# Performance work log

Hardware: AMD Instinct MI355X
Metric: run time of the kernel (lower is better)

## Reference

```python
import jax, jax.numpy as jnp
import numpy as np

B, IN, OUT = 8192, 4096, 2048  # OUT must equal 32*64 per betta/gamma sizes


def setup_inputs() -> dict:
    key = jax.random.key(0)
    kx, kw = jax.random.split(key, 2)
    X = jax.random.normal(kx, (B, IN), dtype=jnp.float32)
    # xavier-uniform-like init for W
    limit = float(np.sqrt(6.0 / (IN + OUT)))
    W = jax.random.uniform(kw, (IN, OUT), minval=-limit, maxval=limit, dtype=jnp.float32)
    absmean = jnp.abs(W).mean(axis=0)
    alpha = jnp.abs(W).mean()          # scalar, >= 0
    betta = absmean[:32]               # (32,), >= 0
    gamma = absmean[32:96]             # (64,), >= 0
    return {"X": X, "W": W, "alpha": alpha, "betta": betta, "gamma": gamma}


def reference(X, W, alpha, betta, gamma):
    # module applies relu_ to alpha/betta/gamma data before the functional call
    alpha = jax.nn.relu(alpha)
    betta = jax.nn.relu(betta)
    gamma = jax.nn.relu(gamma)
    X_bin = jnp.sign(X)                # (B, IN)
    W_bin = jnp.sign(W)                # (IN, OUT)
    # scale[i*64+j] = alpha * betta[i] * gamma[j] -> (OUT,)
    scale = (alpha * jnp.outer(betta, gamma)).reshape(-1)
    return (X_bin @ W_bin) * scale     # (B, OUT)
```

## Files before the change

kernel.cpp:

```cpp
#include <hip/hip_runtime.h>


#define M_DIM 8192
#define K_DIM 4096
#define N_DIM 2048
#define NT    (K_DIM / 256)
#define TILE_BYTES 32768
#define PANEL_BYTES (NT * TILE_BYTES)

typedef int i32x4 __attribute__((ext_vector_type(4)));
typedef int i32x8 __attribute__((ext_vector_type(8)));
typedef float f32x16 __attribute__((ext_vector_type(16)));

__device__ __forceinline__ unsigned int nib4(float x) {
  unsigned int s = (__float_as_uint(x) >> 28) & 0x8u;
  return x == 0.0f ? 0u : (0x2u | s);
}

__device__ __forceinline__ unsigned int pack8(const float* f) {
  unsigned int p = 0;
#pragma unroll
  for (int j = 0; j < 8; ++j) p |= nib4(f[j]) << (4 * j);
  return p;
}

__device__ __forceinline__ void gload_lds16(const void* g, void* lds) {
  __builtin_amdgcn_global_load_lds(
      (const __attribute__((address_space(1))) unsigned int*)g,
      (__attribute__((address_space(3))) unsigned int*)lds, 16, 0, 0);
}

__device__ __forceinline__ i32x8 pad8(i32x4 v) {
  i32x8 r;
  r[0] = v[0]; r[1] = v[1]; r[2] = v[2]; r[3] = v[3];
  r[4] = 0; r[5] = 0; r[6] = 0; r[7] = 0;
  return r;
}

__global__ __launch_bounds__(256) void binX_kernel(
    const float* __restrict__ X, unsigned char* __restrict__ Xq) {
  __shared__ float tile[32][260];
  const int t = threadIdx.x;
  const int rg = blockIdx.x >> 4;
  const int kt = blockIdx.x & 15;
  const int lrow = t >> 6;
  const int col4 = (t & 63) * 4;
#pragma unroll
  for (int i = 0; i < 8; ++i)
    *(float4*)&tile[i * 4 + lrow][col4] =
        *(const float4*)&X[(size_t)(rg * 32 + i * 4 + lrow) * K_DIM + kt * 256 + col4];
  __syncthreads();
  const int s = t >> 5;
  const int r = t & 31;
  float f[32];
#pragma unroll
  for (int j = 0; j < 32; ++j) f[j] = tile[r][s * 32 + j];
  uint4 gq;
  gq.x = pack8(f + 0);  gq.y = pack8(f + 8);
  gq.z = pack8(f + 16); gq.w = pack8(f + 24);
  const int row = rg * 32 + r;
  unsigned char* dst = Xq + (size_t)(row >> 8) * PANEL_BYTES + kt * TILE_BYTES +
                       ((size_t)s * 256 + (row & 255)) * 16;
  *(uint4*)dst = gq;
}

__global__ __launch_bounds__(256) void binW_kernel(
    const float* __restrict__ W, unsigned char* __restrict__ Wq) {
  __shared__ float tile[32][260];
  const int t = threadIdx.x;
  const int q = blockIdx.x >> 7;
  const int kt = (blockIdx.x >> 3) & 15;
  const int s = blockIdx.x & 7;
#pragma unroll
  for (int i = 0; i < 8; ++i) {
    int row = i * 4 + (t >> 6);
    int col4 = (t & 63) * 4;
    *(float4*)&tile[row][col4] =
        *(const float4*)&W[(size_t)(kt * 256 + s * 32 + row) * N_DIM + q * 256 + col4];
  }
  __syncthreads();
  float f[32];
#pragma unroll
  for (int k = 0; k < 32; ++k) f[k] = tile[k][t];
  uint4 gq;
  gq.x = pack8(f + 0);  gq.y = pack8(f + 8);
  gq.z = pack8(f + 16); gq.w = pack8(f + 24);
  unsigned char* dst = Wq + (size_t)q * PANEL_BYTES + kt * TILE_BYTES +
                       ((size_t)s * 256 + t) * 16;
  *(uint4*)dst = gq;
}

__device__ __forceinline__ void stage_tile(const unsigned char* __restrict__ src,
                                           unsigned char* lds, int t) {
#pragma unroll
  for (int p = 0; p < 4; ++p) {
    int c = p * 512 + t;
    gload_lds16(src + c * 16, lds + c * 16);
  }
}

__device__ __forceinline__ void load_frags(i32x4* a4, i32x4* b4,
                                           const unsigned char* pA,
                                           const unsigned char* pB,
                                           int g, int wr, int wc, int l31) {
#pragma unroll
  for (int fm = 0; fm < 4; ++fm)
    a4[fm] = *(const i32x4*)&pA[(g * 256 + wr * 128 + fm * 32 + l31) * 16];
#pragma unroll
  for (int fn = 0; fn < 2; ++fn)
    b4[fn] = *(const i32x4*)&pB[(g * 256 + wc * 64 + fn * 32 + l31) * 16];
}

__global__ __launch_bounds__(512, 2) void gemm_fp4_kernel(
    const unsigned char* __restrict__ Aq,
    const unsigned char* __restrict__ Bq,
    const float* __restrict__ alpha,
    const float* __restrict__ betta,
    const float* __restrict__ gamma,
    float* __restrict__ C) {
  __shared__ __align__(16) unsigned char smem[131072];

  const int t = threadIdx.x;
  const int lane = t & 63;
  const int l31 = lane & 31;
  const int lhi = lane >> 5;
  const int w = t >> 6;
  const int wr = w >> 2;
  const int wc = w & 3;

  const int bid = blockIdx.x;
  const int bm = (bid & 7) * 4 + (bid >> 6);
  const int bn = (bid >> 3) & 7;
  const int row0 = bm * 256;
  const int col0 = bn * 256;

  const unsigned char* Abase = Aq + (size_t)bm * PANEL_BYTES;
  const unsigned char* Bbase = Bq + (size_t)bn * PANEL_BYTES;

  f32x16 acc[4][2];
#pragma unroll
  for (int fm = 0; fm < 4; ++fm)
#pragma unroll
    for (int fn = 0; fn < 2; ++fn)
#pragma unroll
      for (int r = 0; r < 16; ++r) acc[fm][fn][r] = 0.f;

  stage_tile(Abase, &smem[0], t);
  stage_tile(Bbase, &smem[32768], t);
  asm volatile("s_waitcnt vmcnt(0)" ::: "memory");
  __builtin_amdgcn_s_barrier();

  i32x4 a4[2][4], b4[2][2];
  load_frags(a4[0], b4[0], &smem[0], &smem[32768], lhi, wr, wc, l31);

  for (int kt = 0; kt < NT; ++kt) {
    const int cur = kt & 1;
    const unsigned char* pA = &smem[cur * 65536];
    const unsigned char* pB = pA + 32768;

#pragma unroll
    for (int kk = 0; kk < 4; ++kk) {
      const int pb = kk & 1, pn = pb ^ 1;
      asm volatile("s_waitcnt lgkmcnt(0)" ::: "memory");
      __builtin_amdgcn_sched_barrier(0);
      if (kk == 0 && kt + 1 < NT) {
        stage_tile(Abase + (kt + 1) * TILE_BYTES, &smem[(cur ^ 1) * 65536], t);
        stage_tile(Bbase + (kt + 1) * TILE_BYTES, &smem[(cur ^ 1) * 65536 + 32768], t);
      }
      if (kk < 3)
        load_frags(a4[pn], b4[pn], pA, pB, (kk + 1) * 2 + lhi, wr, wc, l31);
      __builtin_amdgcn_sched_barrier(0);
      __builtin_amdgcn_s_setprio(1);
#pragma unroll
      for (int fm = 0; fm < 4; ++fm) {
        i32x8 av = pad8(a4[pb][fm]);
#pragma unroll
        for (int fn = 0; fn < 2; ++fn)
          acc[fm][fn] = __builtin_amdgcn_mfma_scale_f32_32x32x64_f8f6f4(
              av, pad8(b4[pb][fn]), acc[fm][fn], 4, 4,
              0, 0x7F7F7F7F, 0, 0x7F7F7F7F);
      }
      __builtin_amdgcn_s_setprio(0);
    }
    asm volatile("s_waitcnt vmcnt(0)" ::: "memory");
    __builtin_amdgcn_s_barrier();
    if (kt + 1 < NT) {
      const unsigned char* nA = &smem[((kt + 1) & 1) * 65536];
      load_frags(a4[0], b4[0], nA, nA + 32768, lhi, wr, wc, l31);
    }
  }

  const float ra = fmaxf(alpha[0], 0.0f);
#pragma unroll
  for (int fn = 0; fn < 2; ++fn) {
    const int col = col0 + wc * 64 + fn * 32 + l31;
    const float sc = ra * fmaxf(betta[col >> 6], 0.0f) * fmaxf(gamma[col & 63], 0.0f);
#pragma unroll
    for (int fm = 0; fm < 4; ++fm) {
      const int rbase = row0 + wr * 128 + fm * 32 + 4 * lhi;
#pragma unroll
      for (int r = 0; r < 16; ++r) {
        const int row = rbase + (r & 3) + 8 * (r >> 2);
        C[(size_t)row * N_DIM + col] = acc[fm][fn][r] * sc;
      }
    }
  }
}

extern "C" void kernel_launch(void* const* d_in, const int* in_sizes, int n_in,
                              void* d_out, int out_size, void* d_ws, size_t ws_size,
                              hipStream_t stream) {
  const float* X = (const float*)d_in[0];
  const float* W = (const float*)d_in[1];
  const float* alpha = (const float*)d_in[2];
  const float* betta = (const float*)d_in[3];
  const float* gamma = (const float*)d_in[4];
  float* out = (float*)d_out;

  unsigned char* Xq = (unsigned char*)d_ws;
  unsigned char* Wq = Xq + (size_t)(M_DIM / 256) * PANEL_BYTES;

  binW_kernel<<<1024, 256, 0, stream>>>(W, Wq);
  binX_kernel<<<4096, 256, 0, stream>>>(X, Xq);
  gemm_fp4_kernel<<<(M_DIM / 256) * (N_DIM / 256), 512, 0, stream>>>(
      Xq, Wq, alpha, betta, gamma, out);
}
```

Measured before the change: 74.93 us.

## Shrink GEMM block tile to 256x128 with 128-deep K stages

The FP4 GEMM now uses 256-thread blocks computing a 256x128 output tile instead of 512-thread blocks over 256x256. Each K stage covers 128 instead of 256, and LDS usage drops from 128KB to 48KB. The binarized W layout is re-packed into 128-column panels to match, and the grid doubles to 512 blocks. The aim is more resident blocks and better CU fill, traded for more total A-panel reads and more barriers per K step. The binX LDS reads are also vectorized to float4.

Result: no change. 74.55 us (-0.5%).

```diff
diff --git a/kernel.cpp b/kernel.cpp
--- a/kernel.cpp
+++ b/kernel.cpp
@@ -4,9 +4,11 @@
 #define M_DIM 8192
 #define K_DIM 4096
 #define N_DIM 2048
-#define NT    (K_DIM / 256)
-#define TILE_BYTES 32768
-#define PANEL_BYTES (NT * TILE_BYTES)
+#define NT2   (K_DIM / 128)
+#define PANEL_A (128 * 256 * 16)
+#define PANEL_B (128 * 128 * 16)
+#define ATILE 16384
+#define BTILE 8192
 
 typedef int i32x4 __attribute__((ext_vector_type(4)));
 typedef int i32x8 __attribute__((ext_vector_type(8)));
@@ -42,25 +44,27 @@
   __shared__ float tile[32][260];
   const int t = threadIdx.x;
   const int rg = blockIdx.x >> 4;
-  const int kt = blockIdx.x & 15;
+  const int kc = blockIdx.x & 15;
   const int lrow = t >> 6;
   const int col4 = (t & 63) * 4;
 #pragma unroll
   for (int i = 0; i < 8; ++i)
     *(float4*)&tile[i * 4 + lrow][col4] =
-        *(const float4*)&X[(size_t)(rg * 32 + i * 4 + lrow) * K_DIM + kt * 256 + col4];
+        *(const float4*)&X[(size_t)(rg * 32 + i * 4 + lrow) * K_DIM + kc * 256 + col4];
   __syncthreads();
   const int s = t >> 5;
   const int r = t & 31;
   float f[32];
 #pragma unroll
-  for (int j = 0; j < 32; ++j) f[j] = tile[r][s * 32 + j];
+  for (int q = 0; q < 8; ++q)
+    *(float4*)&f[q * 4] = *(const float4*)&tile[r][s * 32 + q * 4];
   uint4 gq;
   gq.x = pack8(f + 0);  gq.y = pack8(f + 8);
   gq.z = pack8(f + 16); gq.w = pack8(f + 24);
   const int row = rg * 32 + r;
-  unsigned char* dst = Xq + (size_t)(row >> 8) * PANEL_BYTES + kt * TILE_BYTES +
-                       ((size_t)s * 256 + (row & 255)) * 16;
+  const int kslot = kc * 8 + s;
+  unsigned char* dst = Xq + (size_t)(row >> 8) * PANEL_A +
+                       ((size_t)kslot * 256 + (row & 255)) * 16;
   *(uint4*)dst = gq;
 }
 
@@ -85,17 +89,25 @@
   uint4 gq;
   gq.x = pack8(f + 0);  gq.y = pack8(f + 8);
   gq.z = pack8(f + 16); gq.w = pack8(f + 24);
-  unsigned char* dst = Wq + (size_t)q * PANEL_BYTES + kt * TILE_BYTES +
-                       ((size_t)s * 256 + t) * 16;
+  const int n = q * 256 + t;
+  const int kslot = kt * 8 + s;
+  unsigned char* dst = Wq + (size_t)(n >> 7) * PANEL_B +
+                       ((size_t)kslot * 128 + (n & 127)) * 16;
   *(uint4*)dst = gq;
 }
 
-__device__ __forceinline__ void stage_tile(const unsigned char* __restrict__ src,
-                                           unsigned char* lds, int t) {
+__device__ __forceinline__ void stage_tiles(const unsigned char* __restrict__ Asrc,
+                                            const unsigned char* __restrict__ Bsrc,
+                                            unsigned char* ldsA, int t) {
 #pragma unroll
   for (int p = 0; p < 4; ++p) {
-    int c = p * 512 + t;
-    gload_lds16(src + c * 16, lds + c * 16);
+    int c = p * 256 + t;
+    gload_lds16(Asrc + c * 16, ldsA + c * 16);
+  }
+#pragma unroll
+  for (int p = 0; p < 2; ++p) {
+    int c = p * 256 + t;
+    gload_lds16(Bsrc + c * 16, ldsA + 16384 + c * 16);
   }
 }
 
@@ -108,34 +120,35 @@
     a4[fm] = *(const i32x4*)&pA[(g * 256 + wr * 128 + fm * 32 + l31) * 16];
 #pragma unroll
   for (int fn = 0; fn < 2; ++fn)
-    b4[fn] = *(const i32x4*)&pB[(g * 256 + wc * 64 + fn * 32 + l31) * 16];
-}
-
-__global__ __launch_bounds__(512, 2) void gemm_fp4_kernel(
+    b4[fn] = *(const i32x4*)&pB[(g * 128 + wc * 64 + fn * 32 + l31) * 16];
+}
+
+__global__ __launch_bounds__(256, 2) void gemm_fp4_kernel(
     const unsigned char* __restrict__ Aq,
     const unsigned char* __restrict__ Bq,
     const float* __restrict__ alpha,
     const float* __restrict__ betta,
     const float* __restrict__ gamma,
     float* __restrict__ C) {
-  __shared__ __align__(16) unsigned char smem[131072];
+  __shared__ __align__(16) unsigned char smem[49152];
 
   const int t = threadIdx.x;
   const int lane = t & 63;
   const int l31 = lane & 31;
   const int lhi = lane >> 5;
   const int w = t >> 6;
-  const int wr = w >> 2;
-  const int wc = w & 3;
+  const int wr = w >> 1;
+  const int wc = w & 1;
 
   const int bid = blockIdx.x;
-  const int bm = (bid & 7) * 4 + (bid >> 6);
-  const int bn = (bid >> 3) & 7;
+  const int j = bid >> 3;
+  const int bm = (bid & 7) * 4 + (j & 3);
+  const int bn = j >> 2;
   const int row0 = bm * 256;
-  const int col0 = bn * 256;
-
-  const unsigned char* Abase = Aq + (size_t)bm * PANEL_BYTES;
-  const unsigned char* Bbase = Bq + (size_t)bn * PANEL_BYTES;
+  const int col0 = bn * 128;
+
+  const unsigned char* Abase = Aq + (size_t)bm * PANEL_A;
+  const unsigned char* Bbase = Bq + (size_t)bn * PANEL_B;
 
   f32x16 acc[4][2];
 #pragma unroll
@@ -145,48 +158,56 @@
 #pragma unroll
       for (int r = 0; r < 16; ++r) acc[fm][fn][r] = 0.f;
 
-  stage_tile(Abase, &smem[0], t);
-  stage_tile(Bbase, &smem[32768], t);
+  stage_tiles(Abase, Bbase, &smem[0], t);
   asm volatile("s_waitcnt vmcnt(0)" ::: "memory");
   __builtin_amdgcn_s_barrier();
 
   i32x4 a4[2][4], b4[2][2];
-  load_frags(a4[0], b4[0], &smem[0], &smem[32768], lhi, wr, wc, l31);
-
-  for (int kt = 0; kt < NT; ++kt) {
+  load_frags(a4[0], b4[0], &smem[0], &smem[16384], lhi, wr, wc, l31);
+
+  for (int kt = 0; kt < NT2; ++kt) {
     const int cur = kt & 1;
-    const unsigned char* pA = &smem[cur * 65536];
-    const unsigned char* pB = pA + 32768;
-
-#pragma unroll
-    for (int kk = 0; kk < 4; ++kk) {
-      const int pb = kk & 1, pn = pb ^ 1;
-      asm volatile("s_waitcnt lgkmcnt(0)" ::: "memory");
-      __builtin_amdgcn_sched_barrier(0);
-      if (kk == 0 && kt + 1 < NT) {
-        stage_tile(Abase + (kt + 1) * TILE_BYTES, &smem[(cur ^ 1) * 65536], t);
-        stage_tile(Bbase + (kt + 1) * TILE_BYTES, &smem[(cur ^ 1) * 65536 + 32768], t);
-      }
-      if (kk < 3)
-        load_frags(a4[pn], b4[pn], pA, pB, (kk + 1) * 2 + lhi, wr, wc, l31);
-      __builtin_amdgcn_sched_barrier(0);
-      __builtin_amdgcn_s_setprio(1);
-#pragma unroll
-      for (int fm = 0; fm < 4; ++fm) {
-        i32x8 av = pad8(a4[pb][fm]);
-#pragma unroll
-        for (int fn = 0; fn < 2; ++fn)
-          acc[fm][fn] = __builtin_amdgcn_mfma_scale_f32_32x32x64_f8f6f4(
-              av, pad8(b4[pb][fn]), acc[fm][fn], 4, 4,
-              0, 0x7F7F7F7F, 0, 0x7F7F7F7F);
-      }
-      __builtin_amdgcn_s_setprio(0);
-    }
+    const unsigned char* pA = &smem[cur * 24576];
+    const unsigned char* pB = pA + 16384;
+
+    asm volatile("s_waitcnt lgkmcnt(0)" ::: "memory");
+    __builtin_amdgcn_sched_barrier(0);
+    if (kt + 1 < NT2)
+      stage_tiles(Abase + (kt + 1) * ATILE, Bbase + (kt + 1) * BTILE,
+                  &smem[(cur ^ 1) * 24576], t);
+    load_frags(a4[1], b4[1], pA, pB, 2 + lhi, wr, wc, l31);
+    __builtin_amdgcn_sched_barrier(0);
+    __builtin_amdgcn_s_setprio(1);
+#pragma unroll
+    for (int fm = 0; fm < 4; ++fm) {
+      i32x8 av = pad8(a4[0][fm]);
+#pragma unroll
+      for (int fn = 0; fn < 2; ++fn)
+        acc[fm][fn] = __builtin_amdgcn_mfma_scale_f32_32x32x64_f8f6f4(
+            av, pad8(b4[0][fn]), acc[fm][fn], 4, 4,
+            0, 0x7F7F7F7F, 0, 0x7F7F7F7F);
+    }
+    __builtin_amdgcn_s_setprio(0);
+
+    asm volatile("s_waitcnt lgkmcnt(0)" ::: "memory");
+    __builtin_amdgcn_sched_barrier(0);
+    __builtin_amdgcn_s_setprio(1);
+#pragma unroll
+    for (int fm = 0; fm < 4; ++fm) {
+      i32x8 av = pad8(a4[1][fm]);
+#pragma unroll
+      for (int fn = 0; fn < 2; ++fn)
+        acc[fm][fn] = __builtin_amdgcn_mfma_scale_f32_32x32x64_f8f6f4(
+            av, pad8(b4[1][fn]), acc[fm][fn], 4, 4,
+            0, 0x7F7F7F7F, 0, 0x7F7F7F7F);
+    }
+    __builtin_amdgcn_s_setprio(0);
+
     asm volatile("s_waitcnt vmcnt(0)" ::: "memory");
     __builtin_amdgcn_s_barrier();
-    if (kt + 1 < NT) {
-      const unsigned char* nA = &smem[((kt + 1) & 1) * 65536];
-      load_frags(a4[0], b4[0], nA, nA + 32768, lhi, wr, wc, l31);
+    if (kt + 1 < NT2) {
+      const unsigned char* nA = &smem[((kt + 1) & 1) * 24576];
+      load_frags(a4[0], b4[0], nA, nA + 16384, lhi, wr, wc, l31);
     }
   }
 
@@ -218,10 +239,10 @@
   float* out = (float*)d_out;
 
   unsigned char* Xq = (unsigned char*)d_ws;
-  unsigned char* Wq = Xq + (size_t)(M_DIM / 256) * PANEL_BYTES;
+  unsigned char* Wq = Xq + (size_t)(M_DIM / 256) * PANEL_A;
 
   binW_kernel<<<1024, 256, 0, stream>>>(W, Wq);
   binX_kernel<<<4096, 256, 0, stream>>>(X, Xq);
-  gemm_fp4_kernel<<<(M_DIM / 256) * (N_DIM / 256), 512, 0, stream>>>(
+  gemm_fp4_kernel<<<(M_DIM / 256) * (N_DIM / 128), 256, 0, stream>>>(
       Xq, Wq, alpha, betta, gamma, out);
 }
```
